# Kernel tuning notes

Measured on AMD Instinct MI355X. Metric: run time of the kernel, lower is better.

The kernel has to match this reference:

```python
import jax, jax.numpy as jnp
import numpy as np

P = 30          # points per cloud (nr_points)
K = 20          # knn neighbors (k)
KS = 5          # spline kernel size (control points)
FN = 10         # filter_nr
EPS = 1e-8


def setup_inputs() -> dict:
    key = jax.random.key(0)
    ks = jax.random.split(key, 7)
    B = 16384
    pos = jax.random.normal(ks[0], (B * P, 3), dtype=jnp.float32)
    W = jax.random.normal(ks[1], (KS, FN), dtype=jnp.float32) * 0.5
    b_dsc = jnp.zeros((FN,), dtype=jnp.float32)
    w1 = jax.random.normal(ks[2], (FN, 256), dtype=jnp.float32) * (1.0 / np.sqrt(FN))
    b1 = jnp.zeros((256,), dtype=jnp.float32)
    w2 = jax.random.normal(ks[3], (256, 40), dtype=jnp.float32) * (1.0 / np.sqrt(256.0))
    b2 = jnp.zeros((40,), dtype=jnp.float32)
    return {"pos": pos, "W": W, "b_dsc": b_dsc, "w1": w1, "b1": b1, "w2": w2, "b2": b2}


def _dsc(pos, W, b_dsc):
    # pos: [N,3] -> per-point directional spline conv features [N, FN]
    B = pos.shape[0] // P
    p = pos.reshape(B, P, 3)
    # knn within each cloud (loop=False): pairwise sq dists, mask self
    d2 = jnp.sum((p[:, :, None, :] - p[:, None, :, :]) ** 2, axis=-1)  # [B,P,P]
    d2 = d2 + jnp.eye(P, dtype=d2.dtype) * 1e10
    _, idx = jax.lax.top_k(-d2, K)  # [B,P,K] nearest neighbor indices
    nb = jax.vmap(lambda pts, ii: pts[ii])(p, idx)  # [B,P,K,3] gather
    rel = nb - p[:, :, None, :]                      # [B,P,K,3]
    # normalize neighborhood into unit ball
    norm = jnp.sqrt(jnp.sum(rel * rel, axis=-1) + EPS)      # [B,P,K]
    scale = jnp.max(norm, axis=-1, keepdims=True) + EPS     # [B,P,1]
    rel_n = rel / scale[..., None]
    # dominant local direction via power iteration on 3x3 covariance
    C = jnp.einsum('bpki,bpkj->bpij', rel_n, rel_n)  # [B,P,3,3]
    v = jnp.ones((B, P, 3), dtype=pos.dtype) / jnp.sqrt(3.0)
    for _ in range(8):
        v = jnp.einsum('bpij,bpj->bpi', C, v)
        v = v / (jnp.sqrt(jnp.sum(v * v, axis=-1, keepdims=True)) + EPS)
    # directional coordinate in [-1,1] -> spline parameter in [0, KS-1]
    t = jnp.einsum('bpki,bpi->bpk', rel_n, v)        # [B,P,K]
    u = jnp.clip((t + 1.0) * 0.5, 0.0, 1.0) * (KS - 1)
    i0 = jnp.clip(jnp.floor(u), 0, KS - 2).astype(jnp.int32)  # [B,P,K]
    frac = (u - i0.astype(u.dtype))[..., None]                 # [B,P,K,1]
    feat = W[i0] * (1.0 - frac) + W[i0 + 1] * frac             # [B,P,K,FN]
    y = jnp.mean(feat, axis=2) + b_dsc                         # [B,P,FN]
    return y.reshape(B * P, FN)


def reference(pos, W, b_dsc, w1, b1, w2, b2):
    y = _dsc(pos, W, b_dsc)                  # [N, FN]
    y = jax.nn.sigmoid(y)
    ys = y.reshape(-1, P, FN).mean(axis=1)   # [B, FN]
    h = jax.nn.elu(ys @ w1 + b1)             # [B, 256]
    logits = h @ w2 + b2                     # [B, 40]
    return jax.nn.log_softmax(logits, axis=1)
```

## Files before the change

kernel.cpp:

```cpp
#include <hip/hip_runtime.h>
#include <math.h>

#define NP 30
#define KNN 20
#define KS 5
#define FN 10
#define EPS 1e-8f
#define CPB 8
#define T1 256

typedef __attribute__((ext_vector_type(8))) short short8v;
typedef __attribute__((ext_vector_type(4))) float float4v;

__device__ __forceinline__ float satf(float x) {
    return fminf(fmaxf(x, 0.0f), 1.0f);
}
__device__ __forceinline__ unsigned short bf16r(float f) {
    unsigned u = __float_as_uint(f);
    u += 0x7fffu + ((u >> 16) & 1u);
    return (unsigned short)(u >> 16);
}
__device__ __forceinline__ float rlanef(float v, int l) {
    return __int_as_float(__builtin_amdgcn_readlane(__float_as_int(v), l));
}
__device__ __forceinline__ int hA_idx(int row, int col) {
    return row * 256 + ((((col >> 3) ^ (row & 7)) << 3) | (col & 7));
}
__device__ __forceinline__ float packdi(float d2, int j) {
    return __uint_as_float((__float_as_uint(d2) & ~31u) | (unsigned)j);
}

__global__ __launch_bounds__(T1, 7) void fused_kernel(
    const float* __restrict__ pos,
    const float* __restrict__ W,
    const float* __restrict__ b_dsc,
    const float* __restrict__ w1,
    const float* __restrict__ b1,
    const float* __restrict__ w2,
    const float* __restrict__ b2,
    float* __restrict__ out,
    int B)
{
    __shared__ float4 ptsF[CPB * NP];
    __shared__ float sbuf[CPB * NP][FN + 1];
    __shared__ float wS[KS * FN];
    __shared__ float bS[FN];
    __shared__ float ysS[CPB * FN];
    __shared__ __align__(16) unsigned short hA[16 * 256];
    __shared__ float Lg[CPB][48];

    const int tid  = threadIdx.x;
    const int base = blockIdx.x * CPB;
    const int w    = tid >> 6;
    const int lane = tid & 63;

    {
        const int lim = min(CPB * NP * 3, B * NP * 3 - base * NP * 3);
        for (int d = tid; d < lim; d += T1) {
            float v  = pos[(size_t)base * (NP * 3) + d];
            int   pt = d / 3;
            ((float*)&ptsF[pt])[d - pt * 3] = v;
        }
    }
    if (tid < KS * FN) wS[tid] = W[tid];
    if (tid < FN)      bS[tid] = b_dsc[tid];
    __syncthreads();

    const int c = tid / NP;
    const int i = tid - c * NP;
    const bool active = (tid < CPB * NP) && (base + c < B);

    if (active) {
        const float4* cp = &ptsF[c * NP];
        const float4 own = cp[i];
        const float ox = own.x, oy = own.y, oz = own.z;

        float vals[32];
        float cxx=0.f, cxy=0.f, cxz=0.f, cyy=0.f, cyz=0.f, czz=0.f;
        #pragma unroll
        for (int j = 0; j < NP; ++j) {
            float4 q = cp[j];
            float dx = q.x - ox, dy = q.y - oy, dz = q.z - oz;
            float d2 = fmaf(dz, dz, fmaf(dy, dy, dx * dx));
            vals[j] = packdi(d2, j);
            cxx = fmaf(dx, dx, cxx); cxy = fmaf(dx, dy, cxy); cxz = fmaf(dx, dz, cxz);
            cyy = fmaf(dy, dy, cyy); cyz = fmaf(dy, dz, cyz); czz = fmaf(dz, dz, czz);
            if ((j % 5) == 4) asm volatile("" ::: "memory");
        }
        vals[30] = packdi(1e11f, 30);
        vals[31] = packdi(1e11f, 31);

        #pragma unroll
        for (int k = 2; k <= 16; k <<= 1) {
            #pragma unroll
            for (int jj = k >> 1; jj > 0; jj >>= 1) {
                #pragma unroll
                for (int tt = 0; tt < 32; ++tt) {
                    int l = tt ^ jj;
                    if (l > tt) {
                        float a  = vals[tt], b = vals[l];
                        float lo = fminf(a, b), hi = fmaxf(a, b);
                        if ((tt & k) == 0) { vals[tt] = lo; vals[l] = hi; }
                        else               { vals[tt] = hi; vals[l] = lo; }
                    }
                }
            }
        }
        #pragma unroll
        for (int q = 0; q < 16; ++q) {
            float a = vals[q], b = vals[16 + q];
            vals[q] = fminf(a, b); vals[16 + q] = fmaxf(a, b);
        }
        #pragma unroll
        for (int jj = 8; jj > 0; jj >>= 1) {
            #pragma unroll
            for (int tt = 16; tt < 32; ++tt) {
                int l = tt ^ jj;
                if (l > tt) {
                    float a = vals[tt], b = vals[l];
                    vals[tt] = fminf(a, b); vals[l] = fmaxf(a, b);
                }
            }
        }
        const float thr_d2 = __uint_as_float(__float_as_uint(vals[20]) & ~31u);
        const float scale  = sqrtf(thr_d2 + EPS) + EPS;
        const float inv_s  = __builtin_amdgcn_rcpf(scale);

        unsigned excl = 0u;
        #pragma unroll
        for (int q = 21; q < 30; ++q) {
            unsigned bq  = __float_as_uint(vals[q]);
            int      idx = (int)(bq & 31u);
            float4 p = cp[idx];
            float dx = p.x - ox, dy = p.y - oy, dz = p.z - oz;
            cxx = fmaf(-dx, dx, cxx); cxy = fmaf(-dx, dy, cxy); cxz = fmaf(-dx, dz, cxz);
            cyy = fmaf(-dy, dy, cyy); cyz = fmaf(-dy, dz, cyz); czz = fmaf(-dz, dz, czz);
            excl |= (1u << idx);
        }

        float tr = cxx + cyy + czz + 1e-30f;
        float rt = __builtin_amdgcn_rcpf(tr);
        float xx = cxx*rt, xy = cxy*rt, xz = cxz*rt;
        float yy = cyy*rt, yz = cyz*rt, zz = czz*rt;
        #pragma unroll
        for (int it = 0; it < 3; ++it) {
            float nxx = fmaf(xx, xx, fmaf(xy, xy, xz * xz));
            float nxy = fmaf(xy, xx + yy, xz * yz);
            float nxz = fmaf(xz, xx + zz, xy * yz);
            float nyy = fmaf(xy, xy, fmaf(yy, yy, yz * yz));
            float nyz = fmaf(yz, yy + zz, xy * xz);
            float nzz = fmaf(xz, xz, fmaf(yz, yz, zz * zz));
            xx = nxx; xy = nxy; xz = nxz; yy = nyy; yz = nyz; zz = nzz;
        }
        float vx = xx + xy + xz;
        float vy = xy + yy + yz;
        float vz = xz + yz + zz;
        float nn = fmaf(vz, vz, fmaf(vy, vy, vx * vx)) + 1e-30f;
        float rr2 = __builtin_amdgcn_rsqf(nn) * inv_s * 2.0f;
        const float wax = vx * rr2, way = vy * rr2, waz = vz * rr2;

        asm volatile("" ::: "memory");

        float a0 = 0.f, a1 = 0.f, a3 = 0.f, s1 = 0.f;
        #pragma unroll 5
        for (int j = 0; j < NP; ++j) {
            float4 q = cp[j];
            float dx = q.x - ox, dy = q.y - oy, dz = q.z - oz;
            float ur = fmaf(dz, waz, fmaf(dy, way, fmaf(dx, wax, 2.0f)));
            float u  = ((excl >> j) & 1u) ? 2.0f : ur;
            a0 += satf(1.0f - fabsf(u));
            a1 += satf(1.0f - fabsf(u - 1.0f));
            a3 += satf(1.0f - fabsf(u - 3.0f));
            s1 += u;
        }
        const float P  = 30.0f - a0 - a1 - a3;
        const float Q  = s1 - a1 - 3.0f * a3;
        const float a4 = fmaf(0.5f, Q, -P);
        const float a2 = P - a4 - 10.0f;

        #pragma unroll
        for (int f = 0; f < FN; ++f) {
            float acc = fmaf(a0, wS[0*FN+f],
                        fmaf(a1, wS[1*FN+f],
                        fmaf(a2, wS[2*FN+f],
                        fmaf(a3, wS[3*FN+f],
                             a4 * wS[4*FN+f]))));
            float y = fmaf(acc, 1.0f / (float)KNN, bS[f]);
            sbuf[tid][f] = __builtin_amdgcn_rcpf(1.0f + __expf(-y));
        }
    }
    __syncthreads();

    if (tid < CPB * FN) {
        int c2 = tid / FN;
        int f  = tid - c2 * FN;
        float s = 0.0f;
        #pragma unroll
        for (int jj = 0; jj < NP; ++jj) s += sbuf[c2 * NP + jj][f];
        ysS[tid] = (base + c2 < B) ? s * (1.0f / (float)NP) : 0.0f;
        (void)f;
    }
    {
        short8v z = {0, 0, 0, 0, 0, 0, 0, 0};
        *(short8v*)&hA[(8 + (tid >> 5)) * 256 + (tid & 31) * 8] = z;
    }
    __syncthreads();

    {
        float ya = ysS[lane];
        float yb = ysS[64 + (lane & 15)];
        float wv[FN];
        #pragma unroll
        for (int f = 0; f < FN; ++f) wv[f] = w1[f * 256 + tid];
        float bb = b1[tid];
        #pragma unroll
        for (int cc = 0; cc < CPB; ++cc) {
            float acc = bb;
            #pragma unroll
            for (int f = 0; f < FN; ++f) {
                const int flat = cc * FN + f;
                float yv = (flat < 64) ? rlanef(ya, flat) : rlanef(yb, flat - 64);
                acc = fmaf(yv, wv[f], acc);
            }
            float h = acc > 0.0f ? acc : __expf(acc) - 1.0f;
            hA[hA_idx(cc, tid)] = bf16r(h);
        }
    }
    __syncthreads();

    if (w < 3) {
        const int  n   = w * 16 + (lane & 15);
        const bool nok = n < 40;
        const int  kg  = (lane >> 4) * 8;
        float4v acc = {0.f, 0.f, 0.f, 0.f};
        #pragma unroll
        for (int s = 0; s < 8; ++s) {
            short8v bfr;
            #pragma unroll
            for (int j = 0; j < 8; ++j) {
                float f = nok ? w2[(s * 32 + kg + j) * 40 + n] : 0.0f;
                bfr[j] = (short)bf16r(f);
            }
            short8v a = *(const short8v*)&hA[hA_idx(lane & 15, kg + s * 32)];
            acc = __builtin_amdgcn_mfma_f32_16x16x32_bf16(a, bfr, acc, 0, 0, 0);
        }
        if (nok) {
            const float bc = b2[n];
            const int   r0 = (lane >> 4) * 4;
            #pragma unroll
            for (int r = 0; r < 4; ++r) {
                int rr = r0 + r;
                if (rr < CPB) Lg[rr][n] = acc[r] + bc;
            }
        }
    }
    __syncthreads();

    if (tid < CPB * 16) {
        int cl = tid >> 4, l = tid & 15;
        float v0 = Lg[cl][l];
        float v1 = Lg[cl][l + 16];
        float v2 = (l < 8) ? Lg[cl][l + 32] : -INFINITY;
        float m = fmaxf(fmaxf(v0, v1), v2);
        #pragma unroll
        for (int msk = 1; msk < 16; msk <<= 1) m = fmaxf(m, __shfl_xor(m, msk));
        float e = __expf(v0 - m) + __expf(v1 - m) + ((l < 8) ? __expf(v2 - m) : 0.0f);
        #pragma unroll
        for (int msk = 1; msk < 16; msk <<= 1) e += __shfl_xor(e, msk);
        float ls = m + __logf(e);
        int cloud = base + cl;
        if (cloud < B) {
            float* op = out + (size_t)cloud * 40;
            op[l]      = v0 - ls;
            op[16 + l] = v1 - ls;
            if (l < 8) op[32 + l] = v2 - ls;
        }
    }
}

extern "C" void kernel_launch(void* const* d_in, const int* in_sizes, int n_in,
                              void* d_out, int out_size, void* d_ws, size_t ws_size,
                              hipStream_t stream) {
    const float* pos   = (const float*)d_in[0];
    const float* W     = (const float*)d_in[1];
    const float* b_dsc = (const float*)d_in[2];
    const float* w1    = (const float*)d_in[3];
    const float* b1    = (const float*)d_in[4];
    const float* w2    = (const float*)d_in[5];
    const float* b2    = (const float*)d_in[6];

    const int N = in_sizes[0] / 3;
    const int B = N / NP;

    const int grid = (B + CPB - 1) / CPB;
    fused_kernel<<<grid, T1, 0, stream>>>(pos, W, b_dsc, w1, b1, w2, b2,
                                          (float*)d_out, B);
}
```

Baseline: 33.37 us.

## Compute kNN keys via norm expansion and covariance from per-cloud moment sums

Stores each point's squared norm alongside its coordinates and ranks neighbors by |q|^2 - 2 q·o, dropping the per-pair difference vectors. The covariance over all points is rebuilt from per-cloud sums of outer products and coordinates, reduced cooperatively in shared memory, instead of each thread accumulating six products per pair. The sigmoid constants are folded into the spline weights and bias so exp2 can be used directly. This trades per-thread ALU work for two extra block barriers and a small shared reduction, and the expanded-distance form can lose floating-point precision, which may change neighbor selection in near ties.

```diff
diff --git a/kernel.cpp b/kernel.cpp
--- a/kernel.cpp
+++ b/kernel.cpp
@@ -26,8 +26,8 @@
 __device__ __forceinline__ int hA_idx(int row, int col) {
     return row * 256 + ((((col >> 3) ^ (row & 7)) << 3) | (col & 7));
 }
-__device__ __forceinline__ float packdi(float d2, int j) {
-    return __uint_as_float((__float_as_uint(d2) & ~31u) | (unsigned)j);
+__device__ __forceinline__ float packdi(float v, int j) {
+    return __uint_as_float((__float_as_uint(v) & ~31u) | (unsigned)j);
 }
 
 __global__ __launch_bounds__(T1, 7) void fused_kernel(
@@ -42,7 +42,8 @@
     int B)
 {
     __shared__ float4 ptsF[CPB * NP];
-    __shared__ float sbuf[CPB * NP][FN + 1];
+    __shared__ float sb[CPB * NP][11];
+    __shared__ __align__(16) float Gs[CPB][12];
     __shared__ float wS[KS * FN];
     __shared__ float bS[FN];
     __shared__ float ysS[CPB * FN];
@@ -54,37 +55,43 @@
     const int w    = tid >> 6;
     const int lane = tid & 63;
 
-    {
-        const int lim = min(CPB * NP * 3, B * NP * 3 - base * NP * 3);
-        for (int d = tid; d < lim; d += T1) {
-            float v  = pos[(size_t)base * (NP * 3) + d];
-            int   pt = d / 3;
-            ((float*)&ptsF[pt])[d - pt * 3] = v;
-        }
-    }
-    if (tid < KS * FN) wS[tid] = W[tid];
-    if (tid < FN)      bS[tid] = b_dsc[tid];
+    if (tid < CPB * NP) {
+        int gp = base * NP + tid;
+        if (gp < B * NP) {
+            const float* pp = pos + (size_t)gp * 3;
+            float x = pp[0], y = pp[1], z = pp[2];
+            float n2 = fmaf(z, z, fmaf(y, y, x * x));
+            ptsF[tid] = make_float4(x, y, z, n2);
+        } else {
+            ptsF[tid] = make_float4(0.f, 0.f, 0.f, 0.f);
+        }
+    }
+    if (tid < KS * FN) wS[tid] = W[tid] * (-0.07213475204444817f);
+    if (tid < FN)      bS[tid] = b_dsc[tid] * (-1.4426950408889634f);
     __syncthreads();
 
     const int c = tid / NP;
     const int i = tid - c * NP;
     const bool active = (tid < CPB * NP) && (base + c < B);
 
+    float vals[32];
+    float ox = 0.f, oy = 0.f, oz = 0.f, oo = 0.f;
+
     if (active) {
         const float4* cp = &ptsF[c * NP];
-        const float4 own = cp[i];
-        const float ox = own.x, oy = own.y, oz = own.z;
-
-        float vals[32];
-        float cxx=0.f, cxy=0.f, cxz=0.f, cyy=0.f, cyz=0.f, czz=0.f;
+        float4 own = cp[i];
+        ox = own.x; oy = own.y; oz = own.z; oo = own.w;
+
+        sb[tid][0] = ox * ox; sb[tid][1] = ox * oy; sb[tid][2] = ox * oz;
+        sb[tid][3] = oy * oy; sb[tid][4] = oy * oz; sb[tid][5] = oz * oz;
+        sb[tid][6] = ox;      sb[tid][7] = oy;     sb[tid][8] = oz;
+
         #pragma unroll
         for (int j = 0; j < NP; ++j) {
             float4 q = cp[j];
-            float dx = q.x - ox, dy = q.y - oy, dz = q.z - oz;
-            float d2 = fmaf(dz, dz, fmaf(dy, dy, dx * dx));
-            vals[j] = packdi(d2, j);
-            cxx = fmaf(dx, dx, cxx); cxy = fmaf(dx, dy, cxy); cxz = fmaf(dx, dz, cxz);
-            cyy = fmaf(dy, dy, cyy); cyz = fmaf(dy, dz, cyz); czz = fmaf(dz, dz, czz);
+            float dt = fmaf(q.z, oz, fmaf(q.y, oy, q.x * ox));
+            float key = fmaf(-2.0f, dt, q.w);
+            vals[j] = packdi(key, j);
             if ((j % 5) == 4) asm volatile("" ::: "memory");
         }
         vals[30] = packdi(1e11f, 30);
@@ -122,14 +129,46 @@
                 }
             }
         }
-        const float thr_d2 = __uint_as_float(__float_as_uint(vals[20]) & ~31u);
-        const float scale  = sqrtf(thr_d2 + EPS) + EPS;
-        const float inv_s  = __builtin_amdgcn_rcpf(scale);
+    }
+    __syncthreads();
+
+    if (tid >= T1 - 72) {
+        int r    = tid - (T1 - 72);
+        int cc   = r / 9;
+        int comp = r - cc * 9;
+        if (base + cc < B) {
+            float s = 0.0f;
+            #pragma unroll
+            for (int k = 0; k < NP; ++k) s += sb[cc * NP + k][comp];
+            Gs[cc][comp] = s;
+        }
+    }
+    __syncthreads();
+
+    if (active) {
+        const float4* cp = &ptsF[c * NP];
+        const float thr_key = __uint_as_float(__float_as_uint(vals[20]) & ~31u);
+        const float thr_d2  = thr_key + oo;
+        const float scale   = sqrtf(thr_d2 + EPS) + EPS;
+        const float inv_s   = __builtin_amdgcn_rcpf(scale);
+
+        float4 g0 = *(const float4*)&Gs[c][0];
+        float4 g1 = *(const float4*)&Gs[c][4];
+        float  sx = g1.z, sy = g1.w, sz = Gs[c][8];
+        float ax = fmaf(30.f, ox, -sx);
+        float ay = fmaf(30.f, oy, -sy);
+        float az = fmaf(30.f, oz, -sz);
+        float cxx = fmaf(ox, ax, fmaf(-sx, ox, g0.x));
+        float cxy = fmaf(oy, ax, fmaf(-sy, ox, g0.y));
+        float cxz = fmaf(oz, ax, fmaf(-sz, ox, g0.z));
+        float cyy = fmaf(oy, ay, fmaf(-sy, oy, g0.w));
+        float cyz = fmaf(oz, ay, fmaf(-sz, oy, g1.x));
+        float czz = fmaf(oz, az, fmaf(-sz, oz, g1.y));
 
         unsigned excl = 0u;
         #pragma unroll
-        for (int q = 21; q < 30; ++q) {
-            unsigned bq  = __float_as_uint(vals[q]);
+        for (int q2 = 21; q2 < 30; ++q2) {
+            unsigned bq  = __float_as_uint(vals[q2]);
             int      idx = (int)(bq & 31u);
             float4 p = cp[idx];
             float dx = p.x - ox, dy = p.y - oy, dz = p.z - oz;
@@ -158,15 +197,13 @@
         float nn = fmaf(vz, vz, fmaf(vy, vy, vx * vx)) + 1e-30f;
         float rr2 = __builtin_amdgcn_rsqf(nn) * inv_s * 2.0f;
         const float wax = vx * rr2, way = vy * rr2, waz = vz * rr2;
-
-        asm volatile("" ::: "memory");
+        const float c0  = 2.0f - fmaf(oz, waz, fmaf(oy, way, ox * wax));
 
         float a0 = 0.f, a1 = 0.f, a3 = 0.f, s1 = 0.f;
         #pragma unroll 5
         for (int j = 0; j < NP; ++j) {
             float4 q = cp[j];
-            float dx = q.x - ox, dy = q.y - oy, dz = q.z - oz;
-            float ur = fmaf(dz, waz, fmaf(dy, way, fmaf(dx, wax, 2.0f)));
+            float ur = fmaf(q.z, waz, fmaf(q.y, way, fmaf(q.x, wax, c0)));
             float u  = ((excl >> j) & 1u) ? 2.0f : ur;
             a0 += satf(1.0f - fabsf(u));
             a1 += satf(1.0f - fabsf(u - 1.0f));
@@ -185,20 +222,18 @@
                         fmaf(a2, wS[2*FN+f],
                         fmaf(a3, wS[3*FN+f],
                              a4 * wS[4*FN+f]))));
-            float y = fmaf(acc, 1.0f / (float)KNN, bS[f]);
-            sbuf[tid][f] = __builtin_amdgcn_rcpf(1.0f + __expf(-y));
+            float z2 = acc + bS[f];
+            sb[tid][f] = __builtin_amdgcn_rcpf(1.0f + exp2f(z2));
         }
     }
     __syncthreads();
 
     if (tid < CPB * FN) {
         int c2 = tid / FN;
-        int f  = tid - c2 * FN;
         float s = 0.0f;
         #pragma unroll
-        for (int jj = 0; jj < NP; ++jj) s += sbuf[c2 * NP + jj][f];
+        for (int jj = 0; jj < NP; ++jj) s += sb[c2 * NP + jj][tid - c2 * FN];
         ysS[tid] = (base + c2 < B) ? s * (1.0f / (float)NP) : 0.0f;
-        (void)f;
     }
     {
         short8v z = {0, 0, 0, 0, 0, 0, 0, 0};
```

Result: faster. 32.68 us (-2.1%).
